# Optimization experiments

Measured on AMD Instinct MI355X. Metric: run time of the kernel, lower is better.

The kernel has to match this reference:

```python
import jax, jax.numpy as jnp
import numpy as np

N = 150000
C_IN = 32
F_OUT = 32
GRID = 256  # linearization stride; > max coordinate (127) + kernel extent
K = 27      # 3x3x3 kernel elements


def _calculate_grid_np(in_pos):
    # Faithful numpy port of calculate_grid: offsets [i-2, j-2, k-2] for i,j,k in 0..2,
    # keep rows with min coord >= 0, dedup with unique (lexicographically sorted).
    ii, jj, kk = np.meshgrid(np.arange(3), np.arange(3), np.arange(3), indexing='ij')
    offs = np.stack([ii, jj, kk], -1).reshape(-1, 3) - 2  # {-2,-1,0}^3
    out = (in_pos[:, None, :].astype(np.int64) + offs[None]).reshape(-1, 3)
    out = out[out.min(1) >= 0]
    return np.unique(out, axis=0)


def _lin(pos):
    # linearize integer voxel coords; fits in int32 for GRID=256
    p = pos.astype(jnp.int32)
    return (p[..., 0] * GRID + p[..., 1]) * GRID + p[..., 2]


def setup_inputs() -> dict:
    key = jax.random.key(0)
    kf, kp, kw = jax.random.split(key, 3)
    features = jax.random.normal(kf, (N, C_IN), jnp.float32)
    in_positions = jax.random.randint(kp, (N, 3), 0, 128, jnp.int32)
    out_positions = jnp.asarray(_calculate_grid_np(np.asarray(in_positions)), jnp.int32)
    fan_in = K * C_IN
    W = jax.random.normal(kw, (K, C_IN, F_OUT), jnp.float32) * np.float32(np.sqrt(2.0 / fan_in))
    return {"features": features, "in_positions": in_positions,
            "out_positions": out_positions, "W": W}


def reference(features, in_positions, out_positions, W):
    # Sparse 3x3x3 conv: out[q] = sum_{d in {0,1,2}^3} W[d] @ feat[q + d]
    # (out active set = in_pos + {-2,-1,0}^3, so taps are d = in - out in {0,1,2}^3)
    M = out_positions.shape[0]
    lid_out = _lin(out_positions)                      # [M], sorted (np.unique is lexicographic)
    d = jnp.stack(jnp.meshgrid(jnp.arange(3), jnp.arange(3), jnp.arange(3),
                               indexing='ij'), -1).reshape(-1, 3)  # [27,3] taps
    lid_in = _lin(in_positions)                        # [N]
    lid_t = lid_in[None, :] - _lin(d)[:, None]         # [27, N] target out cell per (tap, point)
    inb = jnp.all(in_positions[None, :, :] >= d[:, None, :], axis=-1)  # out coords >= 0
    idx = jnp.clip(jnp.searchsorted(lid_out, lid_t), 0, M - 1)         # [27, N]
    valid = inb & (lid_out[idx] == lid_t)
    msgs = jnp.einsum('nc,kcf->knf', features, W)      # [27, N, F]
    msgs = jnp.where(valid[..., None], msgs, jnp.zeros((), features.dtype))
    out = jnp.zeros((M, W.shape[-1]), features.dtype)
    out = out.at[idx.reshape(-1)].add(msgs.reshape(-1, W.shape[-1]))
    return out
```

## Files before the change

kernel.cpp:

```cpp
#include <hip/hip_runtime.h>


#define CELLS (1 << 21)

typedef _Float16 half8 __attribute__((ext_vector_type(8)));

__global__ void claim_k(const int* __restrict__ ipos, int* __restrict__ itable, int N) {
    int n = blockIdx.x * blockDim.x + threadIdx.x;
    if (n >= N) return;
    int x = ipos[3 * n], y = ipos[3 * n + 1], z = ipos[3 * n + 2];
    atomicCAS(&itable[(x << 14) | (y << 7) | z], -1, n);
}

__global__ void count_k(const int* __restrict__ itable, int* __restrict__ blockcnt) {
    __shared__ int wsum[16];
    int cell = blockIdx.x * 1024 + threadIdx.x;
    unsigned long long m = __ballot(itable[cell] >= 0);
    int w = threadIdx.x >> 6;
    if ((threadIdx.x & 63) == 0) wsum[w] = __popcll(m);
    __syncthreads();
    if (threadIdx.x == 0) {
        int s = 0;
        for (int i = 0; i < 16; ++i) s += wsum[i];
        blockcnt[blockIdx.x] = s;
    }
}

__global__ void scan_k(const int* __restrict__ blockcnt, int* __restrict__ blockbase,
                       int* __restrict__ totalbuf) {
    __shared__ int sc[1024];
    int t = threadIdx.x;
    int c0 = blockcnt[2 * t], c1 = blockcnt[2 * t + 1];
    int s = c0 + c1;
    sc[t] = s;
    __syncthreads();
    for (int off = 1; off < 1024; off <<= 1) {
        int v = (t >= off) ? sc[t - off] : 0;
        __syncthreads();
        sc[t] += v;
        __syncthreads();
    }
    int excl = sc[t] - s;
    blockbase[2 * t] = excl;
    blockbase[2 * t + 1] = excl + c0;
    if (t == 1023) totalbuf[0] = sc[t];
}

__global__ void assign_k(const int* __restrict__ itable, const int* __restrict__ blockbase,
                         int* __restrict__ dtable, int* __restrict__ ownerof) {
    __shared__ int wsum[16];
    int cell = blockIdx.x * 1024 + threadIdx.x;
    int owner = itable[cell];
    bool occ = owner >= 0;
    unsigned long long m = __ballot(occ);
    int lane = threadIdx.x & 63, w = threadIdx.x >> 6;
    if (lane == 0) wsum[w] = __popcll(m);
    __syncthreads();
    int woff = 0;
    for (int i = 0; i < w; ++i) woff += wsum[i];
    int dense = blockbase[blockIdx.x] + woff + __popcll(m & ((1ull << lane) - 1));
    dtable[cell] = occ ? dense : -1;
    if (occ) ownerof[dense] = owner;
}

__global__ void copy_k(const int* __restrict__ ownerof, const float* __restrict__ feat,
                       float* __restrict__ featd, const int* __restrict__ totalbuf, int N) {
    int gid = blockIdx.x * blockDim.x + threadIdx.x;
    int d = gid >> 5;
    if (d >= totalbuf[0]) return;
    featd[gid] = feat[(ownerof[d] << 5) + (gid & 31)];
}

__global__ void dup_k(const int* __restrict__ ipos, const int* __restrict__ itable,
                      const int* __restrict__ dtable, const float* __restrict__ feat,
                      float* __restrict__ featd, int N) {
    int gid = blockIdx.x * blockDim.x + threadIdx.x;
    int n = gid >> 5;
    if (n >= N) return;
    int x = ipos[3 * n], y = ipos[3 * n + 1], z = ipos[3 * n + 2];
    int cell = (x << 14) | (y << 7) | z;
    if (itable[cell] == n) return;
    int c = gid & 31;
    atomicAdd(&featd[(dtable[cell] << 5) + c], feat[(n << 5) + c]);
}

__global__ void __launch_bounds__(1024, 8)
conv_k(const int* __restrict__ opos, const int* __restrict__ dtable,
       const float* __restrict__ featd, const float* __restrict__ W,
       float* __restrict__ out, int M, int CH) {
    __shared__ _Float16 wlds16[27 * 1024];
    __shared__ int srec[16][28];

    for (int i = threadIdx.x; i < 27 * 1024; i += blockDim.x) {
        int k = i >> 10, c = (i >> 5) & 31, f = i & 31;
        int j = (c >> 3) & 1, chh = c >> 4, e = c & 7;
        wlds16[((((k << 1) | j) << 1 | chh) << 8) | (f << 3) | e] = (_Float16)W[i];
    }
    __syncthreads();

    const int lane  = threadIdx.x & 63;
    const int f     = lane & 31;
    const int ch    = lane >> 5;
    const int wslot = threadIdx.x >> 6;
    int* sr = srec[wslot];

    const int dx = lane / 9, dy = (lane / 3) % 3, dz = lane % 3;

    const int swz = ((blockIdx.x & 7) << 6) | (blockIdx.x >> 3);
    const int q0   = swz * CH;
    const int qend = min(q0 + CH, M);

    const half8* wp = (const half8*)wlds16;

    int q = q0 + wslot;
    int pv = -1;
    if (lane < 27 && q < qend) {
        int x = opos[3 * q] + dx, y = opos[3 * q + 1] + dy, z = opos[3 * q + 2] + dz;
        if (((x | y | z) & ~127) == 0) pv = dtable[(x << 14) | (y << 7) | z];
    }

    while (q < qend) {
        int qn = q + 16;
        int pvn = -1;
        if (lane < 27 && qn < qend) {
            int x = opos[3 * qn] + dx, y = opos[3 * qn + 1] + dy, z = opos[3 * qn + 2] + dz;
            if (((x | y | z) & ~127) == 0) pvn = dtable[(x << 14) | (y << 7) | z];
        }

        bool found = pv >= 0;
        unsigned long long m = __ballot(found);
        int cnt = __popcll(m);
        if (found) sr[__popcll(m & ((1ull << lane) - 1))] = pv | (lane << 18);

        float a0 = 0.f, a1 = 0.f, a2 = 0.f, a3 = 0.f;
        for (int r = 0; r < cnt; ++r) {
            int rec = sr[r];
            int n = rec & 0x3FFFF, k = rec >> 18;
            const float4* fr = (const float4*)(featd + (n << 5)) + (ch << 2);
            float4 x0 = fr[0], x1 = fr[1], x2 = fr[2], x3 = fr[3];
            half8 w0 = wp[(k << 7) + lane];
            half8 w1 = wp[(k << 7) + 64 + lane];
            a0 += (float)w0[0] * x0.x; a1 += (float)w0[1] * x0.y;
            a2 += (float)w0[2] * x0.z; a3 += (float)w0[3] * x0.w;
            a0 += (float)w0[4] * x1.x; a1 += (float)w0[5] * x1.y;
            a2 += (float)w0[6] * x1.z; a3 += (float)w0[7] * x1.w;
            a0 += (float)w1[0] * x2.x; a1 += (float)w1[1] * x2.y;
            a2 += (float)w1[2] * x2.z; a3 += (float)w1[3] * x2.w;
            a0 += (float)w1[4] * x3.x; a1 += (float)w1[5] * x3.y;
            a2 += (float)w1[6] * x3.z; a3 += (float)w1[7] * x3.w;
        }
        float s = (a0 + a1) + (a2 + a3);
        s += __shfl_xor(s, 32);
        if (ch == 0) out[(q << 5) + f] = s;

        q = qn; pv = pvn;
    }
}

extern "C" void kernel_launch(void* const* d_in, const int* in_sizes, int n_in,
                              void* d_out, int out_size, void* d_ws, size_t ws_size,
                              hipStream_t stream) {
    const float* features = (const float*)d_in[0];
    const int* in_pos     = (const int*)d_in[1];
    const int* out_pos    = (const int*)d_in[2];
    const float* W        = (const float*)d_in[3];
    float* out            = (float*)d_out;

    const int N = in_sizes[1] / 3;
    const int M = in_sizes[2] / 3;

    char* p = (char*)d_ws;
    int* itable    = (int*)p;   p += (size_t)CELLS * 4;
    int* dtable    = (int*)p;   p += (size_t)CELLS * 4;
    int* ownerof   = (int*)p;   p += (size_t)N * 4;
    int* blockcnt  = (int*)p;   p += 2048 * 4;
    int* blockbase = (int*)p;   p += 2048 * 4;
    int* totalbuf  = (int*)p;   p += 16;
    float* featd   = (float*)p; p += (size_t)N * 32 * 4;

    hipMemsetAsync(itable, 0xFF, (size_t)CELLS * 4, stream);

    claim_k <<<(N + 255) / 256, 256, 0, stream>>>(in_pos, itable, N);
    count_k <<<CELLS / 1024, 1024, 0, stream>>>(itable, blockcnt);
    scan_k  <<<1, 1024, 0, stream>>>(blockcnt, blockbase, totalbuf);
    assign_k<<<CELLS / 1024, 1024, 0, stream>>>(itable, blockbase, dtable, ownerof);
    copy_k  <<<(N * 32 + 255) / 256, 256, 0, stream>>>(ownerof, features, featd, totalbuf, N);
    dup_k   <<<(N * 32 + 255) / 256, 256, 0, stream>>>(in_pos, itable, dtable, features, featd, N);

    const int CH = (M + 511) / 512;
    conv_k  <<<512, 1024, 0, stream>>>(out_pos, dtable, featd, W, out, M, CH);
}
```

Before: 868.2 us.

## Process two output rows per wavefront in conv kernel, interleaving their neighbor loops

```diff
diff --git a/kernel.cpp b/kernel.cpp
--- a/kernel.cpp
+++ b/kernel.cpp
@@ -84,12 +84,30 @@
     atomicAdd(&featd[(dtable[cell] << 5) + c], feat[(n << 5) + c]);
 }
 
+#define RECBODY(sj, r, A0, A1, A2, A3)                                          \
+    {                                                                           \
+        int rec = sj[r];                                                        \
+        int n = rec & 0x3FFFF, k = rec >> 18;                                   \
+        const float4* fr = (const float4*)(featd + (n << 5)) + (ch << 2);       \
+        float4 x0 = fr[0], x1 = fr[1], x2 = fr[2], x3 = fr[3];                  \
+        half8 w0 = wp[(k << 7) + lane];                                         \
+        half8 w1 = wp[(k << 7) + 64 + lane];                                    \
+        A0 += (float)w0[0] * x0.x; A1 += (float)w0[1] * x0.y;                   \
+        A2 += (float)w0[2] * x0.z; A3 += (float)w0[3] * x0.w;                   \
+        A0 += (float)w0[4] * x1.x; A1 += (float)w0[5] * x1.y;                   \
+        A2 += (float)w0[6] * x1.z; A3 += (float)w0[7] * x1.w;                   \
+        A0 += (float)w1[0] * x2.x; A1 += (float)w1[1] * x2.y;                   \
+        A2 += (float)w1[2] * x2.z; A3 += (float)w1[3] * x2.w;                   \
+        A0 += (float)w1[4] * x3.x; A1 += (float)w1[5] * x3.y;                   \
+        A2 += (float)w1[6] * x3.z; A3 += (float)w1[7] * x3.w;                   \
+    }
+
 __global__ void __launch_bounds__(1024, 8)
 conv_k(const int* __restrict__ opos, const int* __restrict__ dtable,
        const float* __restrict__ featd, const float* __restrict__ W,
        float* __restrict__ out, int M, int CH) {
     __shared__ _Float16 wlds16[27 * 1024];
-    __shared__ int srec[16][28];
+    __shared__ int srec[16][2][28];
 
     for (int i = threadIdx.x; i < 27 * 1024; i += blockDim.x) {
         int k = i >> 10, c = (i >> 5) & 31, f = i & 31;
@@ -101,59 +119,59 @@
     const int lane  = threadIdx.x & 63;
     const int f     = lane & 31;
     const int ch    = lane >> 5;
+    const int plane = lane & 31;
     const int wslot = threadIdx.x >> 6;
-    int* sr = srec[wslot];
-
-    const int dx = lane / 9, dy = (lane / 3) % 3, dz = lane % 3;
-
-    const int swz = ((blockIdx.x & 7) << 6) | (blockIdx.x >> 3);
+    int (*sr)[28] = srec[wslot];
+
+    const int dx = plane / 9, dy = (plane / 3) % 3, dz = plane % 3;
+
+    const int swz  = ((blockIdx.x & 7) << 6) | (blockIdx.x >> 3);
     const int q0   = swz * CH;
     const int qend = min(q0 + CH, M);
 
     const half8* wp = (const half8*)wlds16;
 
-    int q = q0 + wslot;
-    int pv = -1;
-    if (lane < 27 && q < qend) {
-        int x = opos[3 * q] + dx, y = opos[3 * q + 1] + dy, z = opos[3 * q + 2] + dz;
-        if (((x | y | z) & ~127) == 0) pv = dtable[(x << 14) | (y << 7) | z];
-    }
-
-    while (q < qend) {
-        int qn = q + 16;
-        int pvn = -1;
-        if (lane < 27 && qn < qend) {
-            int x = opos[3 * qn] + dx, y = opos[3 * qn + 1] + dy, z = opos[3 * qn + 2] + dz;
-            if (((x | y | z) & ~127) == 0) pvn = dtable[(x << 14) | (y << 7) | z];
+    auto probe = [&](int row) -> int {
+        int pv = -1;
+        if (plane < 27 && row < qend) {
+            int x = opos[3 * row] + dx, y = opos[3 * row + 1] + dy,
+                z = opos[3 * row + 2] + dz;
+            if (((x | y | z) & ~127) == 0) pv = dtable[(x << 14) | (y << 7) | z];
         }
-
-        bool found = pv >= 0;
-        unsigned long long m = __ballot(found);
-        int cnt = __popcll(m);
-        if (found) sr[__popcll(m & ((1ull << lane) - 1))] = pv | (lane << 18);
-
-        float a0 = 0.f, a1 = 0.f, a2 = 0.f, a3 = 0.f;
-        for (int r = 0; r < cnt; ++r) {
-            int rec = sr[r];
-            int n = rec & 0x3FFFF, k = rec >> 18;
-            const float4* fr = (const float4*)(featd + (n << 5)) + (ch << 2);
-            float4 x0 = fr[0], x1 = fr[1], x2 = fr[2], x3 = fr[3];
-            half8 w0 = wp[(k << 7) + lane];
-            half8 w1 = wp[(k << 7) + 64 + lane];
-            a0 += (float)w0[0] * x0.x; a1 += (float)w0[1] * x0.y;
-            a2 += (float)w0[2] * x0.z; a3 += (float)w0[3] * x0.w;
-            a0 += (float)w0[4] * x1.x; a1 += (float)w0[5] * x1.y;
-            a2 += (float)w0[6] * x1.z; a3 += (float)w0[7] * x1.w;
-            a0 += (float)w1[0] * x2.x; a1 += (float)w1[1] * x2.y;
-            a2 += (float)w1[2] * x2.z; a3 += (float)w1[3] * x2.w;
-            a0 += (float)w1[4] * x3.x; a1 += (float)w1[5] * x3.y;
-            a2 += (float)w1[6] * x3.z; a3 += (float)w1[7] * x3.w;
+        return pv;
+    };
+
+    int p  = q0 + (wslot << 1);
+    int pv = probe(p + ch);
+
+    while (p < qend) {
+        int pn  = p + 32;
+        int pvn = probe(pn + ch);
+
+        unsigned long long m = __ballot(pv >= 0);
+        unsigned mlo = (unsigned)m, mhi = (unsigned)(m >> 32);
+        int cnt0 = __popc(mlo), cnt1 = __popc(mhi);
+        if (pv >= 0) {
+            unsigned mh = ch ? mhi : mlo;
+            sr[ch][__popc(mh & ((1u << plane) - 1))] = pv | (plane << 18);
         }
-        float s = (a0 + a1) + (a2 + a3);
-        s += __shfl_xor(s, 32);
-        if (ch == 0) out[(q << 5) + f] = s;
-
-        q = qn; pv = pvn;
+
+        float a00 = 0.f, a01 = 0.f, a02 = 0.f, a03 = 0.f;
+        float a10 = 0.f, a11 = 0.f, a12 = 0.f, a13 = 0.f;
+        int mx = (cnt0 > cnt1) ? cnt0 : cnt1;
+        for (int r = 0; r < mx; ++r) {
+            if (r < cnt0) RECBODY(sr[0], r, a00, a01, a02, a03);
+            if (r < cnt1) RECBODY(sr[1], r, a10, a11, a12, a13);
+        }
+
+        float s0 = (a00 + a01) + (a02 + a03);
+        s0 += __shfl_xor(s0, 32);
+        float s1 = (a10 + a11) + (a12 + a13);
+        s1 += __shfl_xor(s1, 32);
+        int row = p + ch;
+        if (row < qend) out[(row << 5) + f] = ch ? s1 : s0;
+
+        p = pn; pv = pvn;
     }
 }
 
```

Measured after the change: 836.4 us. 1.04x faster.
